# Optimization experiments

Measured on AMD Instinct MI355X. Metric: run time of the kernel, lower is better.

The kernel has to match this reference:

```python
import jax, jax.numpy as jnp
import numpy as np

B, N, C, H, E, K = 2, 2048, 1024, 4096, 8, 2
TAU = 1.0


def setup_inputs() -> dict:
    key = jax.random.key(0)
    ks = jax.random.split(key, 9)
    x = jax.random.normal(ks[0], (B, N, C), dtype=jnp.float32)
    T = B * N
    u = jax.random.uniform(ks[1], (T, E), minval=1e-6, maxval=1.0 - 1e-6)
    gumbel_noise = -jnp.log(-jnp.log(u))  # Gumbel(0,1) samples
    s = 0.02
    gate_w = jax.random.normal(ks[2], (C, E), dtype=jnp.float32) * s
    gate_b = jnp.zeros((E,), dtype=jnp.float32)
    w1 = jax.random.normal(ks[3], (E, C, H), dtype=jnp.float32) * s
    b1 = jnp.zeros((E, H), dtype=jnp.float32)
    w2 = jax.random.normal(ks[4], (E, H, C), dtype=jnp.float32) * s
    b2 = jnp.zeros((E, C), dtype=jnp.float32)
    return {"x": x, "gumbel_noise": gumbel_noise, "gate_w": gate_w,
            "gate_b": gate_b, "w1": w1, "b1": b1, "w2": w2, "b2": b2}


def reference(x, gumbel_noise, gate_w, gate_b, w1, b1, w2, b2):
    Bb, Nn, Cc = x.shape
    x_flat = x.reshape(-1, Cc)                                  # [T, C]
    logits = x_flat @ gate_w + gate_b                           # [T, E]
    # F.gumbel_softmax(hard=False, tau=1): softmax((logits + g)/tau)
    gates = jax.nn.softmax((logits + gumbel_noise) / TAU, axis=-1)
    mean_gates = gates.mean(axis=0)
    load_balance_loss = jnp.sum(mean_gates * jnp.log(mean_gates + 1e-8))
    topk_vals, topk_idxs = jax.lax.top_k(gates, K)              # [T, K]
    T = x_flat.shape[0]
    # scatter top-k gate weights into a dense [T, E] combine matrix
    comb = jnp.zeros((T, E), dtype=gates.dtype)
    comb = comb.at[jnp.arange(T)[:, None], topk_idxs].set(topk_vals)
    # dense per-expert MLP over all tokens, then weighted combine
    h = jnp.einsum('tc,ech->teh', x_flat, w1) + b1              # [T, E, H]
    h = jax.nn.gelu(h, approximate=False)                        # exact GELU (nn.GELU)
    y = jnp.einsum('teh,ehc->tec', h, w2) + b2                  # [T, E, C]
    out = jnp.einsum('te,tec->tc', comb, y)                     # [T, C]
    return out.reshape(Bb, Nn, Cc), load_balance_loss
```

## Files before the change

### kernel.cpp

```cpp
#include <hip/hip_runtime.h>
#include <math.h>

#define TT  4096
#define CC  1024
#define HH  4096
#define EE  8
#define TKN 8192

typedef _Float16 f16x8 __attribute__((ext_vector_type(8)));
typedef float    f32x4 __attribute__((ext_vector_type(4)));

#define GLD_LDS16(g, l)                                                        \
    __builtin_amdgcn_global_load_lds(                                          \
        (const __attribute__((address_space(1))) void*)(g),                    \
        (__attribute__((address_space(3))) void*)(l), 16, 0, 0)

__global__ __launch_bounds__(256) void gate_kernel(
    const float* __restrict__ x, const float* __restrict__ gn,
    const float* __restrict__ gw, const float* __restrict__ gb,
    int* __restrict__ topk_idx, float* __restrict__ topk_w,
    int* __restrict__ counts, float* __restrict__ gsum)
{
    int wave = threadIdx.x >> 6, lane = threadIdx.x & 63;
    int t = blockIdx.x * 4 + wave;
    const float* xrow = x + (size_t)t * CC;

    double acc[EE];
#pragma unroll
    for (int e = 0; e < EE; e++) acc[e] = 0.0;

#pragma unroll
    for (int i = 0; i < CC / 64; i++) {
        int c = i * 64 + lane;
        float xv = xrow[c];
        const float4* g4 = reinterpret_cast<const float4*>(gw + (size_t)c * EE);
        float4 g0 = g4[0], g1 = g4[1];
        double xd = (double)xv;
        acc[0] += xd * (double)g0.x; acc[1] += xd * (double)g0.y;
        acc[2] += xd * (double)g0.z; acc[3] += xd * (double)g0.w;
        acc[4] += xd * (double)g1.x; acc[5] += xd * (double)g1.y;
        acc[6] += xd * (double)g1.z; acc[7] += xd * (double)g1.w;
    }
#pragma unroll
    for (int e = 0; e < EE; e++)
#pragma unroll
        for (int off = 32; off > 0; off >>= 1)
            acc[e] += __shfl_xor(acc[e], off);

    double z[EE], m = -1e300;
#pragma unroll
    for (int e = 0; e < EE; e++) {
        z[e] = acc[e] + (double)gb[e] + (double)gn[(size_t)t * EE + e];
        m = fmax(m, z[e]);
    }
    double p[EE], s = 0.0;
#pragma unroll
    for (int e = 0; e < EE; e++) { p[e] = exp(z[e] - m); s += p[e]; }
    double inv = 1.0 / s;
    double g[EE];
#pragma unroll
    for (int e = 0; e < EE; e++) g[e] = p[e] * inv;

    int i1 = 0; double v1 = g[0];
#pragma unroll
    for (int e = 1; e < EE; e++) if (g[e] > v1) { v1 = g[e]; i1 = e; }
    int i2 = -1; double v2 = -1.0;
#pragma unroll
    for (int e = 0; e < EE; e++) if (e != i1 && g[e] > v2) { v2 = g[e]; i2 = e; }

    if (lane == 0) {
        topk_idx[t * 2 + 0] = i1; topk_w[t * 2 + 0] = (float)v1;
        topk_idx[t * 2 + 1] = i2; topk_w[t * 2 + 1] = (float)v2;
        atomicAdd(&counts[i1], 1);
        atomicAdd(&counts[i2], 1);
    }

    __shared__ float gp[4][EE];
    if (lane == 0) {
#pragma unroll
        for (int e = 0; e < EE; e++) gp[wave][e] = (float)g[e];
    }
    __syncthreads();
    if (threadIdx.x < EE) {
        float s4 = gp[0][threadIdx.x] + gp[1][threadIdx.x] +
                   gp[2][threadIdx.x] + gp[3][threadIdx.x];
        atomicAdd(&gsum[threadIdx.x], s4);
    }
}

__global__ __launch_bounds__(256) void transpose_f16_kernel(
    const float* __restrict__ src, _Float16* __restrict__ dst, int R, int Ccols)
{
    __shared__ float tile[64][65];
    int e = blockIdx.z;
    const float* s = src + (size_t)e * R * Ccols;
    _Float16* d = dst + (size_t)e * R * Ccols;
    int c0 = blockIdx.x * 64, r0 = blockIdx.y * 64;
    int tid = threadIdx.x;

    int lr = tid >> 4;
    int lc = (tid & 15) * 4;
#pragma unroll
    for (int i = 0; i < 4; i++) {
        int r = lr + i * 16;
        float4 v = *reinterpret_cast<const float4*>(
            s + (size_t)(r0 + r) * Ccols + c0 + lc);
        tile[r][lc + 0] = v.x; tile[r][lc + 1] = v.y;
        tile[r][lc + 2] = v.z; tile[r][lc + 3] = v.w;
    }
    __syncthreads();

    int oc = tid >> 2;
    int orr = (tid & 3) * 16;
    f16x8 o0, o1;
#pragma unroll
    for (int j = 0; j < 8; j++) o0[j] = (_Float16)tile[orr + j][oc];
#pragma unroll
    for (int j = 0; j < 8; j++) o1[j] = (_Float16)tile[orr + 8 + j][oc];
    *reinterpret_cast<f16x8*>(d + (size_t)(c0 + oc) * R + r0 + orr)     = o0;
    *reinterpret_cast<f16x8*>(d + (size_t)(c0 + oc) * R + r0 + orr + 8) = o1;
}

__global__ void scan_kernel(const int* __restrict__ counts, int* __restrict__ offsets,
                            const float* __restrict__ gsum, float* __restrict__ loss_out)
{
    if (threadIdx.x == 0) {
        int o = 0;
#pragma unroll
        for (int e = 0; e < EE; e++) { offsets[e] = o; o += counts[e]; }
        offsets[EE] = o;
        float L = 0.f;
#pragma unroll
        for (int e = 0; e < EE; e++) {
            float me = gsum[e] / (float)TT;
            L += me * logf(me + 1e-8f);
        }
        *loss_out = L;
    }
}

__global__ __launch_bounds__(256) void scatter_kernel(
    const int* __restrict__ topk_idx, const int* __restrict__ offsets,
    int* __restrict__ fill, int* __restrict__ rowtok, int* __restrict__ posmap)
{
    int t = blockIdx.x * 256 + threadIdx.x;
#pragma unroll
    for (int k = 0; k < 2; k++) {
        int e = topk_idx[t * 2 + k];
        int pos = offsets[e] + atomicAdd(&fill[e], 1);
        rowtok[pos] = t;
        posmap[t * 2 + k] = pos;
    }
}

__global__ __launch_bounds__(256) void gather_kernel(
    const float* __restrict__ x, const int* __restrict__ rowtok,
    _Float16* __restrict__ xg)
{
    int p = blockIdx.x * 2 + (threadIdx.x >> 7);
    int c = (threadIdx.x & 127) * 8;
    int t = rowtok[p];
    const float4* s = reinterpret_cast<const float4*>(x + (size_t)t * CC + c);
    float4 v0 = s[0], v1 = s[1];
    f16x8 o;
    o[0] = (_Float16)v0.x; o[1] = (_Float16)v0.y;
    o[2] = (_Float16)v0.z; o[3] = (_Float16)v0.w;
    o[4] = (_Float16)v1.x; o[5] = (_Float16)v1.y;
    o[6] = (_Float16)v1.z; o[7] = (_Float16)v1.w;
    *reinterpret_cast<f16x8*>(xg + (size_t)p * CC + c) = o;
}


__global__ __launch_bounds__(512) void gemm1_kernel(
    const _Float16* __restrict__ xg, const _Float16* __restrict__ w1t,
    const float* __restrict__ b1, const int* __restrict__ offsets,
    _Float16* __restrict__ h)
{
    int GX = gridDim.x, GY = gridDim.y;
    int nwg = GX * GY * (int)gridDim.z;
    int f = blockIdx.x + GX * (blockIdx.y + GY * blockIdx.z);
    int cpx = nwg >> 3;
    f = (f & 7) * cpx + (f >> 3);
    int bx = f % GX; int tq = f / GX; int by = tq % GY; int bz = tq / GY;

    int e = bz;
    int segs = offsets[e];
    int M = offsets[e + 1] - segs;
    int m0 = bx * 256;
    if (m0 >= M) return;
    int n0 = by * 256;

    __shared__ __align__(16) _Float16 As[2][256 * 32];
    __shared__ __align__(16) _Float16 Bs[2][256 * 32];

    int tid = threadIdx.x;
    int wave = tid >> 6, lane = tid & 63;
    int wm = (wave >> 2) * 128, wn = (wave & 3) * 64;
    int lrow = lane & 15;
    int kgx = (lane >> 4) ^ ((lane >> 1) & 3);
    int aoff = (wm + lrow) * 32 + kgx * 8;
    int boff = (wn + lrow) * 32 + kgx * 8;

    const _Float16* wB = w1t + (size_t)e * HH * CC;

    int r = tid >> 2;
    int cc = ((tid & 3) ^ ((tid >> 3) & 3)) * 8;
    int rA0 = m0 + r;       if (rA0 >= M) rA0 = M - 1;
    int rA1 = m0 + 128 + r; if (rA1 >= M) rA1 = M - 1;
    const _Float16* ap0 = xg + (size_t)(segs + rA0) * CC + cc;
    const _Float16* ap1 = xg + (size_t)(segs + rA1) * CC + cc;
    const _Float16* bp0 = wB + (size_t)(n0 + r) * CC + cc;
    const _Float16* bp1 = wB + (size_t)(n0 + 128 + r) * CC + cc;
    int ldst = tid * 8;

    f32x4 acc[8][4];
#pragma unroll
    for (int i = 0; i < 8; i++)
#pragma unroll
        for (int j = 0; j < 4; j++)
#pragma unroll
            for (int q = 0; q < 4; q++) acc[i][j][q] = 0.f;

    auto STAGE = [&](int b) {
        GLD_LDS16(ap0, &As[b][0] + ldst);
        GLD_LDS16(ap1, &As[b][0] + 4096 + ldst);
        GLD_LDS16(bp0, &Bs[b][0] + ldst);
        GLD_LDS16(bp1, &Bs[b][0] + 4096 + ldst);
        ap0 += 32; ap1 += 32; bp0 += 32; bp1 += 32;
    };

    const int NK = CC / 32;
    STAGE(0);
    __syncthreads();
    for (int t = 0; t < NK; ++t) {
        int b = t & 1;
        if (t + 1 < NK) STAGE(b ^ 1);
        const _Float16* Ab = &As[b][0] + aoff;
        const _Float16* Bb = &Bs[b][0] + boff;
        f16x8 aF[4], bF[4];
#pragma unroll
        for (int j = 0; j < 4; j++)
            bF[j] = *reinterpret_cast<const f16x8*>(Bb + j * 512);
#pragma unroll
        for (int i = 0; i < 4; i++)
            aF[i] = *reinterpret_cast<const f16x8*>(Ab + i * 512);
        __builtin_amdgcn_s_setprio(1);
#pragma unroll
        for (int i = 0; i < 4; i++)
#pragma unroll
            for (int j = 0; j < 4; j++)
                acc[i][j] = __builtin_amdgcn_mfma_f32_16x16x32_f16(
                    aF[i], bF[j], acc[i][j], 0, 0, 0);
        __builtin_amdgcn_s_setprio(0);
        __builtin_amdgcn_s_barrier();
#pragma unroll
        for (int i = 0; i < 4; i++)
            aF[i] = *reinterpret_cast<const f16x8*>(Ab + (4 + i) * 512);
        __builtin_amdgcn_s_setprio(1);
#pragma unroll
        for (int i = 0; i < 4; i++)
#pragma unroll
            for (int j = 0; j < 4; j++)
                acc[4 + i][j] = __builtin_amdgcn_mfma_f32_16x16x32_f16(
                    aF[i], bF[j], acc[4 + i][j], 0, 0, 0);
        __builtin_amdgcn_s_setprio(0);
        __syncthreads();
    }

    int rbase = (lane >> 4) * 4;
#pragma unroll
    for (int mi = 0; mi < 8; mi++) {
#pragma unroll
        for (int ni = 0; ni < 4; ni++) {
            int gcol = n0 + wn + ni * 16 + lrow;
            float bias = b1[(size_t)e * HH + gcol];
#pragma unroll
            for (int q = 0; q < 4; q++) {
                int rowl = m0 + wm + mi * 16 + rbase + q;
                if (rowl < M) {
                    float v = acc[mi][ni][q] + bias;
                    v = 0.5f * v * (1.0f + erff(v * 0.70710678118654752f));
                    h[(size_t)(segs + rowl) * HH + gcol] = (_Float16)v;
                }
            }
        }
    }
}

__global__ __launch_bounds__(512) void gemm2_kernel(
    const _Float16* __restrict__ h, const _Float16* __restrict__ w2t,
    const float* __restrict__ b2, const int* __restrict__ offsets,
    float* __restrict__ y)
{
    int GX = gridDim.x, GY = gridDim.y;
    int nwg = GX * GY * (int)gridDim.z;
    int f = blockIdx.x + GX * (blockIdx.y + GY * blockIdx.z);
    int cpx = nwg >> 3;
    f = (f & 7) * cpx + (f >> 3);
    int bx = f % GX; int tq = f / GX; int by = tq % GY; int bz = tq / GY;

    int e = bz;
    int segs = offsets[e];
    int M = offsets[e + 1] - segs;
    int m0 = bx * 128;
    if (m0 >= M) return;
    int kz = by >> 2;
    int n0 = (by & 3) * 256;
    int kbeg = kz * (HH / 2);

    __shared__ __align__(16) _Float16 As[2][128 * 32];
    __shared__ __align__(16) _Float16 Bs[2][256 * 32];

    int tid = threadIdx.x;
    int wave = tid >> 6, lane = tid & 63;
    int wm = (wave >> 2) * 64, wn = (wave & 3) * 64;
    int lrow = lane & 15;
    int kgx = (lane >> 4) ^ ((lane >> 1) & 3);
    int aoff = (wm + lrow) * 32 + kgx * 8;
    int boff = (wn + lrow) * 32 + kgx * 8;

    const _Float16* wB = w2t + (size_t)e * CC * HH;

    int r = tid >> 2;
    int cc = ((tid & 3) ^ ((tid >> 3) & 3)) * 8;
    int rA = m0 + r; if (rA >= M) rA = M - 1;
    const _Float16* ap  = h  + (size_t)(segs + rA) * HH + kbeg + cc;
    const _Float16* bp0 = wB + (size_t)(n0 + r) * HH + kbeg + cc;
    const _Float16* bp1 = wB + (size_t)(n0 + 128 + r) * HH + kbeg + cc;
    int ldst = tid * 8;

    f32x4 acc[4][4];
#pragma unroll
    for (int i = 0; i < 4; i++)
#pragma unroll
        for (int j = 0; j < 4; j++)
#pragma unroll
            for (int q = 0; q < 4; q++) acc[i][j][q] = 0.f;

    auto STAGE = [&](int b) {
        GLD_LDS16(ap,  &As[b][0] + ldst);
        GLD_LDS16(bp0, &Bs[b][0] + ldst);
        GLD_LDS16(bp1, &Bs[b][0] + 4096 + ldst);
        ap += 32; bp0 += 32; bp1 += 32;
    };

    const int NK = (HH / 2) / 32;
    STAGE(0);
    __syncthreads();
    for (int t = 0; t < NK; ++t) {
        int b = t & 1;
        if (t + 1 < NK) STAGE(b ^ 1);
        const _Float16* Ab = &As[b][0] + aoff;
        const _Float16* Bb = &Bs[b][0] + boff;
        f16x8 aF[4], bF[4];
#pragma unroll
        for (int j = 0; j < 4; j++)
            bF[j] = *reinterpret_cast<const f16x8*>(Bb + j * 512);
#pragma unroll
        for (int i = 0; i < 4; i++)
            aF[i] = *reinterpret_cast<const f16x8*>(Ab + i * 512);
        __builtin_amdgcn_s_setprio(1);
#pragma unroll
        for (int i = 0; i < 2; i++)
#pragma unroll
            for (int j = 0; j < 4; j++)
                acc[i][j] = __builtin_amdgcn_mfma_f32_16x16x32_f16(
                    aF[i], bF[j], acc[i][j], 0, 0, 0);
        __builtin_amdgcn_s_setprio(0);
        __builtin_amdgcn_s_barrier();
        __builtin_amdgcn_s_setprio(1);
#pragma unroll
        for (int i = 2; i < 4; i++)
#pragma unroll
            for (int j = 0; j < 4; j++)
                acc[i][j] = __builtin_amdgcn_mfma_f32_16x16x32_f16(
                    aF[i], bF[j], acc[i][j], 0, 0, 0);
        __builtin_amdgcn_s_setprio(0);
        __syncthreads();
    }

    float* yk = y + (size_t)kz * TKN * CC;
    int rbase = (lane >> 4) * 4;
#pragma unroll
    for (int mi = 0; mi < 4; mi++) {
#pragma unroll
        for (int ni = 0; ni < 4; ni++) {
            int gcol = n0 + wn + ni * 16 + lrow;
            float bias = (kz == 0) ? b2[(size_t)e * CC + gcol] : 0.f;
#pragma unroll
            for (int q = 0; q < 4; q++) {
                int rowl = m0 + wm + mi * 16 + rbase + q;
                if (rowl < M)
                    yk[(size_t)(segs + rowl) * CC + gcol] = acc[mi][ni][q] + bias;
            }
        }
    }
}

__global__ __launch_bounds__(256) void combine_kernel(
    const float* __restrict__ y, const int* __restrict__ posmap,
    const float* __restrict__ topk_w, float* __restrict__ out)
{
    int t = blockIdx.x * 2 + (threadIdx.x >> 7);
    int c = (threadIdx.x & 127) * 8;
    int p0 = posmap[t * 2 + 0], p1 = posmap[t * 2 + 1];
    float wa = topk_w[t * 2 + 0], wb = topk_w[t * 2 + 1];
    const float* y1 = y + (size_t)TKN * CC;
    const float4* a0 = reinterpret_cast<const float4*>(y  + (size_t)p0 * CC + c);
    const float4* a1 = reinterpret_cast<const float4*>(y1 + (size_t)p0 * CC + c);
    const float4* b0 = reinterpret_cast<const float4*>(y  + (size_t)p1 * CC + c);
    const float4* b1 = reinterpret_cast<const float4*>(y1 + (size_t)p1 * CC + c);
    float4 r0, r1;
    float4 av0 = a0[0], av1 = a0[1], aw0 = a1[0], aw1 = a1[1];
    float4 bv0 = b0[0], bv1 = b0[1], bw0 = b1[0], bw1 = b1[1];
    r0.x = wa * (av0.x + aw0.x) + wb * (bv0.x + bw0.x);
    r0.y = wa * (av0.y + aw0.y) + wb * (bv0.y + bw0.y);
    r0.z = wa * (av0.z + aw0.z) + wb * (bv0.z + bw0.z);
    r0.w = wa * (av0.w + aw0.w) + wb * (bv0.w + bw0.w);
    r1.x = wa * (av1.x + aw1.x) + wb * (bv1.x + bw1.x);
    r1.y = wa * (av1.y + aw1.y) + wb * (bv1.y + bw1.y);
    r1.z = wa * (av1.z + aw1.z) + wb * (bv1.z + bw1.z);
    r1.w = wa * (av1.w + aw1.w) + wb * (bv1.w + bw1.w);
    float4* o = reinterpret_cast<float4*>(out + (size_t)t * CC + c);
    o[0] = r0; o[1] = r1;
}

extern "C" void kernel_launch(void* const* d_in, const int* in_sizes, int n_in,
                              void* d_out, int out_size, void* d_ws, size_t ws_size,
                              hipStream_t stream)
{
    const float* x  = (const float*)d_in[0];
    const float* gn = (const float*)d_in[1];
    const float* gw = (const float*)d_in[2];
    const float* gb = (const float*)d_in[3];
    const float* w1 = (const float*)d_in[4];
    const float* b1 = (const float*)d_in[5];
    const float* w2 = (const float*)d_in[6];
    const float* b2 = (const float*)d_in[7];
    float* out = (float*)d_out;

    char* w = (char*)d_ws;
    int*   counts  = (int*)(w + 0);
    int*   fill    = (int*)(w + 32);
    int*   offsets = (int*)(w + 64);
    float* gsum    = (float*)(w + 128);
    size_t off = 256;
    int*   topk_idx = (int*)(w + off);   off += (size_t)TT * 2 * 4;
    float* topk_w   = (float*)(w + off); off += (size_t)TT * 2 * 4;
    int*   rowtok   = (int*)(w + off);   off += (size_t)TKN * 4;
    int*   posmap   = (int*)(w + off);   off += (size_t)TKN * 4;
    _Float16* xg  = (_Float16*)(w + off); off += (size_t)TKN * CC * 2;
    _Float16* w1t = (_Float16*)(w + off); off += (size_t)EE * HH * CC * 2;
    _Float16* w2t = (_Float16*)(w + off); off += (size_t)EE * CC * HH * 2;
    _Float16* hbuf = (_Float16*)(w + off); off += (size_t)TKN * HH * 2;
    float* ybuf = (float*)w1t;

    (void)hipMemsetAsync(d_ws, 0, 256, stream);

    gate_kernel<<<TT / 4, 256, 0, stream>>>(x, gn, gw, gb, topk_idx, topk_w,
                                            counts, gsum);
    transpose_f16_kernel<<<dim3(HH / 64, CC / 64, EE), 256, 0, stream>>>(
        w1, w1t, CC, HH);
    transpose_f16_kernel<<<dim3(CC / 64, HH / 64, EE), 256, 0, stream>>>(
        w2, w2t, HH, CC);
    scan_kernel<<<1, 64, 0, stream>>>(counts, offsets, gsum, out + (size_t)TT * CC);
    scatter_kernel<<<TT / 256, 256, 0, stream>>>(topk_idx, offsets, fill,
                                                 rowtok, posmap);
    gather_kernel<<<TKN / 2, 256, 0, stream>>>(x, rowtok, xg);
    gemm1_kernel<<<dim3(6, HH / 256, EE), 512, 0, stream>>>(xg, w1t, b1,
                                                            offsets, hbuf);
    gemm2_kernel<<<dim3(12, 2 * (CC / 256), EE), 512, 0, stream>>>(
        hbuf, w2t, b2, offsets, ybuf);
    combine_kernel<<<TT / 2, 256, 0, stream>>>(ybuf, posmap, topk_w, out);
}
```

Baseline: 825.8 us.

## Widen K-tile to 64 with XOR swizzle and enlarge gemm2 M-tile to 256

Measured after the change: 848.1 us. +2.7%, slower.

```diff
diff --git a/kernel.cpp b/kernel.cpp
--- a/kernel.cpp
+++ b/kernel.cpp
@@ -171,7 +171,7 @@
 }
 
 
-__global__ __launch_bounds__(512) void gemm1_kernel(
+__global__ __launch_bounds__(512, 2) void gemm1_kernel(
     const _Float16* __restrict__ xg, const _Float16* __restrict__ w1t,
     const float* __restrict__ b1, const int* __restrict__ offsets,
     _Float16* __restrict__ h)
@@ -190,28 +190,29 @@
     if (m0 >= M) return;
     int n0 = by * 256;
 
-    __shared__ __align__(16) _Float16 As[2][256 * 32];
-    __shared__ __align__(16) _Float16 Bs[2][256 * 32];
+    __shared__ __align__(16) _Float16 As[2][256 * 64];
+    __shared__ __align__(16) _Float16 Bs[2][256 * 64];
 
     int tid = threadIdx.x;
     int wave = tid >> 6, lane = tid & 63;
     int wm = (wave >> 2) * 128, wn = (wave & 3) * 64;
-    int lrow = lane & 15;
-    int kgx = (lane >> 4) ^ ((lane >> 1) & 3);
-    int aoff = (wm + lrow) * 32 + kgx * 8;
-    int boff = (wn + lrow) * 32 + kgx * 8;
+    int lrow = lane & 15, kg = lane >> 4;
+    int rx = lrow & 7;
 
     const _Float16* wB = w1t + (size_t)e * HH * CC;
 
-    int r = tid >> 2;
-    int cc = ((tid & 3) ^ ((tid >> 3) & 3)) * 8;
-    int rA0 = m0 + r;       if (rA0 >= M) rA0 = M - 1;
-    int rA1 = m0 + 128 + r; if (rA1 >= M) rA1 = M - 1;
-    const _Float16* ap0 = xg + (size_t)(segs + rA0) * CC + cc;
-    const _Float16* ap1 = xg + (size_t)(segs + rA1) * CC + cc;
-    const _Float16* bp0 = wB + (size_t)(n0 + r) * CC + cc;
-    const _Float16* bp1 = wB + (size_t)(n0 + 128 + r) * CC + cc;
-    int ldst = tid * 8;
+    const _Float16* ap[4]; const _Float16* bp[4];
+    int lofs[4];
+#pragma unroll
+    for (int j = 0; j < 4; j++) {
+        int ch = j * 512 + tid;
+        int row = ch >> 3, slot = ch & 7;
+        int col = ((slot ^ (row & 7)) * 8);
+        int rm = m0 + row; if (rm >= M) rm = M - 1;
+        ap[j] = xg + (size_t)(segs + rm) * CC + col;
+        bp[j] = wB + (size_t)(n0 + row) * CC + col;
+        lofs[j] = ch * 8;
+    }
 
     f32x4 acc[8][4];
 #pragma unroll
@@ -222,49 +223,48 @@
             for (int q = 0; q < 4; q++) acc[i][j][q] = 0.f;
 
     auto STAGE = [&](int b) {
-        GLD_LDS16(ap0, &As[b][0] + ldst);
-        GLD_LDS16(ap1, &As[b][0] + 4096 + ldst);
-        GLD_LDS16(bp0, &Bs[b][0] + ldst);
-        GLD_LDS16(bp1, &Bs[b][0] + 4096 + ldst);
-        ap0 += 32; ap1 += 32; bp0 += 32; bp1 += 32;
+#pragma unroll
+        for (int j = 0; j < 4; j++) {
+            GLD_LDS16(ap[j], &As[b][0] + lofs[j]);
+            GLD_LDS16(bp[j], &Bs[b][0] + lofs[j]);
+            ap[j] += 64; bp[j] += 64;
+        }
     };
 
-    const int NK = CC / 32;
+    const int NK = CC / 64;
     STAGE(0);
     __syncthreads();
+    int cur = 0;
     for (int t = 0; t < NK; ++t) {
-        int b = t & 1;
-        if (t + 1 < NK) STAGE(b ^ 1);
-        const _Float16* Ab = &As[b][0] + aoff;
-        const _Float16* Bb = &Bs[b][0] + boff;
-        f16x8 aF[4], bF[4];
-#pragma unroll
-        for (int j = 0; j < 4; j++)
-            bF[j] = *reinterpret_cast<const f16x8*>(Bb + j * 512);
-#pragma unroll
-        for (int i = 0; i < 4; i++)
-            aF[i] = *reinterpret_cast<const f16x8*>(Ab + i * 512);
-        __builtin_amdgcn_s_setprio(1);
-#pragma unroll
-        for (int i = 0; i < 4; i++)
-#pragma unroll
-            for (int j = 0; j < 4; j++)
-                acc[i][j] = __builtin_amdgcn_mfma_f32_16x16x32_f16(
-                    aF[i], bF[j], acc[i][j], 0, 0, 0);
-        __builtin_amdgcn_s_setprio(0);
-        __builtin_amdgcn_s_barrier();
-#pragma unroll
-        for (int i = 0; i < 4; i++)
-            aF[i] = *reinterpret_cast<const f16x8*>(Ab + (4 + i) * 512);
-        __builtin_amdgcn_s_setprio(1);
-#pragma unroll
-        for (int i = 0; i < 4; i++)
-#pragma unroll
-            for (int j = 0; j < 4; j++)
-                acc[4 + i][j] = __builtin_amdgcn_mfma_f32_16x16x32_f16(
-                    aF[i], bF[j], acc[4 + i][j], 0, 0, 0);
-        __builtin_amdgcn_s_setprio(0);
+        if (t + 1 < NK) STAGE(cur ^ 1);
+        const _Float16* Ab = &As[cur][0];
+        const _Float16* Bb = &Bs[cur][0];
+#pragma unroll
+        for (int s = 0; s < 2; s++) {
+            f16x8 aF[8], bF[4];
+#pragma unroll
+            for (int i = 0; i < 8; i++) {
+                int row = wm + i * 16 + lrow;
+                aF[i] = *reinterpret_cast<const f16x8*>(
+                    Ab + row * 64 + (((s * 4 + kg) ^ rx) * 8));
+            }
+#pragma unroll
+            for (int j = 0; j < 4; j++) {
+                int row = wn + j * 16 + lrow;
+                bF[j] = *reinterpret_cast<const f16x8*>(
+                    Bb + row * 64 + (((s * 4 + kg) ^ rx) * 8));
+            }
+            __builtin_amdgcn_s_setprio(1);
+#pragma unroll
+            for (int i = 0; i < 8; i++)
+#pragma unroll
+                for (int j = 0; j < 4; j++)
+                    acc[i][j] = __builtin_amdgcn_mfma_f32_16x16x32_f16(
+                        aF[i], bF[j], acc[i][j], 0, 0, 0);
+            __builtin_amdgcn_s_setprio(0);
+        }
         __syncthreads();
+        cur ^= 1;
     }
 
     int rbase = (lane >> 4) * 4;
@@ -287,7 +287,7 @@
     }
 }
 
-__global__ __launch_bounds__(512) void gemm2_kernel(
+__global__ __launch_bounds__(512, 2) void gemm2_kernel(
     const _Float16* __restrict__ h, const _Float16* __restrict__ w2t,
     const float* __restrict__ b2, const int* __restrict__ offsets,
     float* __restrict__ y)
@@ -302,87 +302,93 @@
     int e = bz;
     int segs = offsets[e];
     int M = offsets[e + 1] - segs;
-    int m0 = bx * 128;
+    int m0 = bx * 256;
     if (m0 >= M) return;
     int kz = by >> 2;
     int n0 = (by & 3) * 256;
     int kbeg = kz * (HH / 2);
 
-    __shared__ __align__(16) _Float16 As[2][128 * 32];
-    __shared__ __align__(16) _Float16 Bs[2][256 * 32];
+    __shared__ __align__(16) _Float16 As[2][256 * 64];
+    __shared__ __align__(16) _Float16 Bs[2][256 * 64];
 
     int tid = threadIdx.x;
     int wave = tid >> 6, lane = tid & 63;
-    int wm = (wave >> 2) * 64, wn = (wave & 3) * 64;
-    int lrow = lane & 15;
-    int kgx = (lane >> 4) ^ ((lane >> 1) & 3);
-    int aoff = (wm + lrow) * 32 + kgx * 8;
-    int boff = (wn + lrow) * 32 + kgx * 8;
+    int wm = (wave >> 2) * 128, wn = (wave & 3) * 64;
+    int lrow = lane & 15, kg = lane >> 4;
+    int rx = lrow & 7;
 
     const _Float16* wB = w2t + (size_t)e * CC * HH;
 
-    int r = tid >> 2;
-    int cc = ((tid & 3) ^ ((tid >> 3) & 3)) * 8;
-    int rA = m0 + r; if (rA >= M) rA = M - 1;
-    const _Float16* ap  = h  + (size_t)(segs + rA) * HH + kbeg + cc;
-    const _Float16* bp0 = wB + (size_t)(n0 + r) * HH + kbeg + cc;
-    const _Float16* bp1 = wB + (size_t)(n0 + 128 + r) * HH + kbeg + cc;
-    int ldst = tid * 8;
-
-    f32x4 acc[4][4];
-#pragma unroll
-    for (int i = 0; i < 4; i++)
+    const _Float16* ap[4]; const _Float16* bp[4];
+    int lofs[4];
+#pragma unroll
+    for (int j = 0; j < 4; j++) {
+        int ch = j * 512 + tid;
+        int row = ch >> 3, slot = ch & 7;
+        int col = ((slot ^ (row & 7)) * 8);
+        int rm = m0 + row; if (rm >= M) rm = M - 1;
+        ap[j] = h  + (size_t)(segs + rm) * HH + kbeg + col;
+        bp[j] = wB + (size_t)(n0 + row) * HH + kbeg + col;
+        lofs[j] = ch * 8;
+    }
+
+    f32x4 acc[8][4];
+#pragma unroll
+    for (int i = 0; i < 8; i++)
 #pragma unroll
         for (int j = 0; j < 4; j++)
 #pragma unroll
             for (int q = 0; q < 4; q++) acc[i][j][q] = 0.f;
 
     auto STAGE = [&](int b) {
-        GLD_LDS16(ap,  &As[b][0] + ldst);
-        GLD_LDS16(bp0, &Bs[b][0] + ldst);
-        GLD_LDS16(bp1, &Bs[b][0] + 4096 + ldst);
-        ap += 32; bp0 += 32; bp1 += 32;
+#pragma unroll
+        for (int j = 0; j < 4; j++) {
+            GLD_LDS16(ap[j], &As[b][0] + lofs[j]);
+            GLD_LDS16(bp[j], &Bs[b][0] + lofs[j]);
+            ap[j] += 64; bp[j] += 64;
+        }
     };
 
-    const int NK = (HH / 2) / 32;
+    const int NK = (HH / 2) / 64;
     STAGE(0);
     __syncthreads();
+    int cur = 0;
     for (int t = 0; t < NK; ++t) {
-        int b = t & 1;
-        if (t + 1 < NK) STAGE(b ^ 1);
-        const _Float16* Ab = &As[b][0] + aoff;
-        const _Float16* Bb = &Bs[b][0] + boff;
-        f16x8 aF[4], bF[4];
-#pragma unroll
-        for (int j = 0; j < 4; j++)
-            bF[j] = *reinterpret_cast<const f16x8*>(Bb + j * 512);
-#pragma unroll
-        for (int i = 0; i < 4; i++)
-            aF[i] = *reinterpret_cast<const f16x8*>(Ab + i * 512);
-        __builtin_amdgcn_s_setprio(1);
-#pragma unroll
-        for (int i = 0; i < 2; i++)
-#pragma unroll
-            for (int j = 0; j < 4; j++)
-                acc[i][j] = __builtin_amdgcn_mfma_f32_16x16x32_f16(
-                    aF[i], bF[j], acc[i][j], 0, 0, 0);
-        __builtin_amdgcn_s_setprio(0);
-        __builtin_amdgcn_s_barrier();
-        __builtin_amdgcn_s_setprio(1);
-#pragma unroll
-        for (int i = 2; i < 4; i++)
-#pragma unroll
-            for (int j = 0; j < 4; j++)
-                acc[i][j] = __builtin_amdgcn_mfma_f32_16x16x32_f16(
-                    aF[i], bF[j], acc[i][j], 0, 0, 0);
-        __builtin_amdgcn_s_setprio(0);
+        if (t + 1 < NK) STAGE(cur ^ 1);
+        const _Float16* Ab = &As[cur][0];
+        const _Float16* Bb = &Bs[cur][0];
+#pragma unroll
+        for (int s = 0; s < 2; s++) {
+            f16x8 aF[8], bF[4];
+#pragma unroll
+            for (int i = 0; i < 8; i++) {
+                int row = wm + i * 16 + lrow;
+                aF[i] = *reinterpret_cast<const f16x8*>(
+                    Ab + row * 64 + (((s * 4 + kg) ^ rx) * 8));
+            }
+#pragma unroll
+            for (int j = 0; j < 4; j++) {
+                int row = wn + j * 16 + lrow;
+                bF[j] = *reinterpret_cast<const f16x8*>(
+                    Bb + row * 64 + (((s * 4 + kg) ^ rx) * 8));
+            }
+            __builtin_amdgcn_s_setprio(1);
+#pragma unroll
+            for (int i = 0; i < 8; i++)
+#pragma unroll
+                for (int j = 0; j < 4; j++)
+                    acc[i][j] = __builtin_amdgcn_mfma_f32_16x16x32_f16(
+                        aF[i], bF[j], acc[i][j], 0, 0, 0);
+            __builtin_amdgcn_s_setprio(0);
+        }
         __syncthreads();
+        cur ^= 1;
     }
 
     float* yk = y + (size_t)kz * TKN * CC;
     int rbase = (lane >> 4) * 4;
 #pragma unroll
-    for (int mi = 0; mi < 4; mi++) {
+    for (int mi = 0; mi < 8; mi++) {
 #pragma unroll
         for (int ni = 0; ni < 4; ni++) {
             int gcol = n0 + wn + ni * 16 + lrow;
@@ -469,7 +475,7 @@
     gather_kernel<<<TKN / 2, 256, 0, stream>>>(x, rowtok, xg);
     gemm1_kernel<<<dim3(6, HH / 256, EE), 512, 0, stream>>>(xg, w1t, b1,
                                                             offsets, hbuf);
-    gemm2_kernel<<<dim3(12, 2 * (CC / 256), EE), 512, 0, stream>>>(
+    gemm2_kernel<<<dim3(6, 2 * (CC / 256), EE), 512, 0, stream>>>(
         hbuf, w2t, b2, offsets, ybuf);
     combine_kernel<<<TT / 2, 256, 0, stream>>>(ybuf, posmap, topk_w, out);
 }
```
